# Kernel tuning notes

Hardware: AMD Instinct MI355X
Metric: run time of the kernel (lower is better)

Reference implementation:

```python
import jax, jax.numpy as jnp
import numpy as np

N_HEAD = 16
R = 8
THRESHOLD = 0.1


def setup_inputs() -> dict:
    key = jax.random.key(0)
    k1, k2, k3 = jax.random.split(key, 3)
    B, T, C = 2, 2048, 2048
    fused_dim = 3 * C  # 2*H*D_std + C + 2*H*R with D_std+R = head_dim
    x = jax.random.normal(k1, (B, T, C), dtype=jnp.float32)
    W_attn = jax.random.normal(k2, (fused_dim, C), dtype=jnp.float32) * (1.0 / np.sqrt(C))
    W_proj = jax.random.normal(k3, (C, C), dtype=jnp.float32) * (1.0 / np.sqrt(C))
    w_std = jnp.ones((N_HEAD,), dtype=jnp.float32) * 0.5
    w_rec = jnp.ones((N_HEAD,), dtype=jnp.float32) * 0.3
    return {"x": x, "W_attn": W_attn, "W_proj": W_proj, "w_std": w_std, "w_rec": w_rec}


def _causal_attention(Q, K, V):
    # Q,K: [B,H,T,D]; V: [B,H,T,Dv]; scale = 1/sqrt(D) (torch SDPA default)
    D = Q.shape[-1]
    scores = jnp.einsum("bhqd,bhkd->bhqk", Q, K) / jnp.sqrt(jnp.asarray(D, Q.dtype))
    T = Q.shape[2]
    causal = jnp.tril(jnp.ones((T, T), dtype=bool))
    scores = jnp.where(causal, scores, jnp.asarray(-jnp.inf, scores.dtype))
    probs = jax.nn.softmax(scores, axis=-1)
    return jnp.einsum("bhqk,bhkd->bhqd", probs, V)


def reference(x, W_attn, W_proj, w_std, w_rec):
    B, T, C = x.shape
    H = N_HEAD
    head_dim = C // H
    D_std = head_dim - R
    q_std_end = H * D_std
    k_std_end = q_std_end + H * D_std
    v_end = k_std_end + C
    q_low_end = v_end + H * R

    fused = jnp.einsum("btc,fc->btf", x, W_attn)  # c_attn, no bias

    def split_heads(a, d):
        return a.reshape(B, T, H, d).transpose(0, 2, 1, 3)  # [B,H,T,d]

    Q_std = split_heads(fused[..., :q_std_end], D_std)
    K_std = split_heads(fused[..., q_std_end:k_std_end], D_std)
    V = split_heads(fused[..., k_std_end:v_end], head_dim)
    Q_low = split_heads(fused[..., v_end:q_low_end], R)
    K_low = split_heads(fused[..., q_low_end:], R)

    # per-head routing: RA heads fold low-rank K/Q cross terms, baseline heads keep standard concat
    use_ra = (w_rec > THRESHOLD).reshape(1, H, 1, 1)
    ws = jnp.sqrt(jnp.clip(w_std, 1e-8, None)).reshape(1, H, 1, 1)
    wr = jnp.sqrt(jnp.clip(w_rec, 1e-8, None)).reshape(1, H, 1, 1)

    Qf_low = jnp.where(use_ra, wr * K_low, ws * Q_low)
    Kf_low = jnp.where(use_ra, wr * Q_low, ws * K_low)
    Qf = jnp.concatenate([ws * Q_std, Qf_low], axis=-1)  # [B,H,T,head_dim]
    Kf = jnp.concatenate([ws * K_std, Kf_low], axis=-1)

    out = _causal_attention(Qf, Kf, V)  # [B,H,T,head_dim]
    out = out.transpose(0, 2, 1, 3).reshape(B, T, C)
    return jnp.einsum("btc,oc->bto", out, W_proj)
```

## Files before the change

kernel.cpp:

```cpp
#include <hip/hip_runtime.h>
#include <math.h>

#define Bb 2
#define Tt 2048
#define Cc 2048
#define Hh 16
#define DH 128
#define FUSED 6144
#define Mm 4096
#define QSC 0.08838834764831845f

typedef __bf16 bf16x8 __attribute__((ext_vector_type(8)));
typedef float  f32x4  __attribute__((ext_vector_type(4)));

__device__ __forceinline__ unsigned short f2bf(float f) {
  unsigned int u = __float_as_uint(f);
  u = (u + 0x7fffu + ((u >> 16) & 1u)) >> 16;
  return (unsigned short)u;
}

__device__ __forceinline__ void gload16(const void* src, void* lds) {
  __builtin_amdgcn_global_load_lds((const __attribute__((address_space(1))) void*)src,
                                   (__attribute__((address_space(3))) void*)lds, 16, 0, 0);
}

__global__ void f2bf_arr(const float* __restrict__ src, unsigned short* __restrict__ dst, int n)
{
  int i = (blockIdx.x * blockDim.x + threadIdx.x) * 4;
  int stride = gridDim.x * blockDim.x * 4;
  for (; i < n; i += stride) {
    float4 v = *(const float4*)&src[i];
    ushort4 o;
    o.x = f2bf(v.x); o.y = f2bf(v.y); o.z = f2bf(v.z); o.w = f2bf(v.w);
    *(ushort4*)&dst[i] = o;
  }
}

template <int MODE>
__global__ __launch_bounds__(256)
void gemm_bf16(const unsigned short* __restrict__ A, const unsigned short* __restrict__ Bw,
               float* __restrict__ out,
               unsigned short* __restrict__ Qb, unsigned short* __restrict__ Kb,
               unsigned short* __restrict__ Vb,
               const float* __restrict__ w_std, const float* __restrict__ w_rec,
               int N, int K)
{
  __shared__ unsigned short As[128 * 64];
  __shared__ unsigned short Bs[128 * 64];
  __shared__ float lws[Hh], lwr[Hh];
  __shared__ int   lra[Hh];

  const int tid  = threadIdx.x;
  const int lane = tid & 63;
  const int w    = tid >> 6;
  const int wr   = w >> 1, wc = w & 1;
  const int lrow = lane & 15, lgrp = lane >> 4;
  const int m0 = blockIdx.y * 128;
  const int n0 = blockIdx.x * 128;

  if (MODE == 1 && tid < Hh) {
    float a = w_std[tid]; lws[tid] = sqrtf(a < 1e-8f ? 1e-8f : a);
    float r = w_rec[tid]; lwr[tid] = sqrtf(r < 1e-8f ? 1e-8f : r);
    lra[tid] = (r > 0.1f) ? 1 : 0;
  }

  f32x4 acc[4][4] = {};

  for (int kt = 0; kt < K; kt += 64) {
#pragma unroll
    for (int c = 0; c < 4; ++c) {
      int base16 = (c * 4 + w) * 64;
      int o16 = base16 + lane;
      int rr = o16 >> 3, cc = o16 & 7;
      int csw = (cc ^ (rr & 7)) << 3;
      gload16(A  + (size_t)(m0 + rr) * K + kt + csw, As + base16 * 8);
      gload16(Bw + (size_t)(n0 + rr) * K + kt + csw, Bs + base16 * 8);
    }
    __syncthreads();

#pragma unroll
    for (int s = 0; s < 2; ++s) {
      bf16x8 af[4], bfr[4];
#pragma unroll
      for (int i = 0; i < 4; ++i) {
        int row = wr * 64 + i * 16 + lrow;
        int ch  = s * 4 + lgrp;
        af[i]  = *(const bf16x8*)&As[row * 64 + ((ch ^ (row & 7)) << 3)];
        int col = wc * 64 + i * 16 + lrow;
        bfr[i] = *(const bf16x8*)&Bs[col * 64 + ((ch ^ (col & 7)) << 3)];
      }
#pragma unroll
      for (int i = 0; i < 4; ++i)
#pragma unroll
        for (int j = 0; j < 4; ++j)
          acc[i][j] = __builtin_amdgcn_mfma_f32_16x16x32_bf16(af[i], bfr[j], acc[i][j], 0, 0, 0);
    }
    __syncthreads();
  }

  if (MODE == 0) {
#pragma unroll
    for (int i = 0; i < 4; ++i)
#pragma unroll
      for (int r = 0; r < 4; ++r) {
        int m = m0 + wr * 64 + i * 16 + lgrp * 4 + r;
#pragma unroll
        for (int j = 0; j < 4; ++j) {
          int n = n0 + wc * 64 + j * 16 + lrow;
          out[(size_t)m * N + n] = acc[i][j][r];
        }
      }
  } else {
#pragma unroll
    for (int i = 0; i < 4; ++i)
#pragma unroll
      for (int r = 0; r < 4; ++r) {
        int m = m0 + wr * 64 + i * 16 + lgrp * 4 + r;
        int b = m >> 11, t = m & 2047;
#pragma unroll
        for (int j = 0; j < 4; ++j) {
          int f = n0 + wc * 64 + j * 16 + lrow;
          float v = acc[i][j][r];
          unsigned short* dst; int h, d; float sc;
          if (f < 1920)      { h = f / 120; d = f - h * 120; dst = Qb; sc = lws[h] * QSC; }
          else if (f < 3840) { int g = f - 1920; h = g / 120; d = g - h * 120; dst = Kb; sc = lws[h]; }
          else if (f < 5888) { int g = f - 3840; h = g >> 7; d = g & 127; dst = Vb; sc = 1.f; }
          else if (f < 6016) { int g = f - 5888; h = g >> 3; d = 120 + (g & 7);
                               if (lra[h]) { dst = Kb; sc = lwr[h]; }
                               else        { dst = Qb; sc = lws[h] * QSC; } }
          else               { int g = f - 6016; h = g >> 3; d = 120 + (g & 7);
                               if (lra[h]) { dst = Qb; sc = lwr[h] * QSC; }
                               else        { dst = Kb; sc = lws[h]; } }
          dst[((((size_t)b * Hh + h) * Tt + t) << 7) + d] = f2bf(v * sc);
        }
      }
  }
}

__global__ __launch_bounds__(256)
void vtrans(const unsigned short* __restrict__ Vb, unsigned short* __restrict__ Vtb)
{
  __shared__ unsigned short Vs[64 * 128];
  const int tid = threadIdx.x;
  const int bh = blockIdx.y, t0 = blockIdx.x * 64;
  const unsigned short* src = Vb + ((size_t)bh * Tt + t0) * DH;
#pragma unroll
  for (int c = 0; c < 4; ++c) {
    int u = c * 256 + tid;
    int row = u >> 4, ch = u & 15;
    *(uint4*)&Vs[row * 128 + ch * 8] = *(const uint4*)&src[(size_t)row * DH + ch * 8];
  }
  __syncthreads();
  unsigned short* dstb = Vtb + (size_t)bh * DH * Tt + t0;
#pragma unroll
  for (int c = 0; c < 4; ++c) {
    int u = c * 256 + tid;
    int d = u & 127, tc = u >> 7;
    unsigned short tmp[8];
#pragma unroll
    for (int j = 0; j < 8; ++j) tmp[j] = Vs[(tc * 8 + j) * 128 + d];
    *(uint4*)&dstb[(size_t)d * Tt + tc * 8] = *(uint4*)tmp;
  }
}

__global__ __launch_bounds__(256)
void attn_mfma(const unsigned short* __restrict__ Qb, const unsigned short* __restrict__ Kb,
               const unsigned short* __restrict__ Vtb, unsigned short* __restrict__ attb)
{
  __shared__ unsigned short Kt[64 * 128];
  __shared__ unsigned short Vt[128 * 64];
  __shared__ unsigned short QP[64 * 128];

  const int tid = threadIdx.x, lane = tid & 63, w = tid >> 6;
  const int lrow = lane & 15, lgrp = lane >> 4;
  const int bh = blockIdx.y;
  const int qt = 31 - blockIdx.x;
  const int q0 = qt * 64;
  const unsigned short* Qh = Qb  + (size_t)bh * Tt * DH;
  const unsigned short* Kh = Kb  + (size_t)bh * Tt * DH;
  const unsigned short* Vh = Vtb + (size_t)bh * DH * Tt;

#pragma unroll
  for (int c = 0; c < 4; ++c) {
    int base16 = (c * 4 + w) * 64;
    int o16 = base16 + lane;
    int rr = o16 >> 4, cc = o16 & 15;
    gload16(Qh + (size_t)(q0 + rr) * DH + ((cc ^ (rr & 7)) << 3), QP + base16 * 8);
  }
  __syncthreads();

  bf16x8 qf[4];
#pragma unroll
  for (int s = 0; s < 4; ++s) {
    int row = w * 16 + lrow;
    int ch  = s * 4 + lgrp;
    qf[s] = *(const bf16x8*)&QP[row * 128 + ((ch ^ (row & 7)) << 3)];
  }
  __syncthreads();

  f32x4 o[8] = {};
  float mrun[4], lrun[4];
#pragma unroll
  for (int r = 0; r < 4; ++r) { mrun[r] = -INFINITY; lrun[r] = 0.f; }
  unsigned short* Pw = QP + w * 1024;

  for (int t = 0; t <= qt; ++t) {
    const int kv0 = t * 64;
#pragma unroll
    for (int c = 0; c < 4; ++c) {
      int base16 = (c * 4 + w) * 64;
      int o16 = base16 + lane;
      { int rr = o16 >> 4, cc = o16 & 15;
        gload16(Kh + (size_t)(kv0 + rr) * DH + ((cc ^ (rr & 7)) << 3), Kt + base16 * 8); }
      { int rr = o16 >> 3, cc = o16 & 7;
        gload16(Vh + (size_t)rr * Tt + kv0 + ((cc ^ (rr & 7)) << 3), Vt + base16 * 8); }
    }
    __syncthreads();

    f32x4 sv[4] = {};
#pragma unroll
    for (int ks = 0; ks < 4; ++ks)
#pragma unroll
      for (int j = 0; j < 4; ++j) {
        int krow = j * 16 + lrow;
        int ch   = ks * 4 + lgrp;
        bf16x8 kf = *(const bf16x8*)&Kt[krow * 128 + ((ch ^ (krow & 7)) << 3)];
        sv[j] = __builtin_amdgcn_mfma_f32_16x16x32_bf16(qf[ks], kf, sv[j], 0, 0, 0);
      }

    float sc[4];
#pragma unroll
    for (int r = 0; r < 4; ++r) {
      if (t == qt) {
        int qrow = q0 + w * 16 + lgrp * 4 + r;
#pragma unroll
        for (int j = 0; j < 4; ++j) {
          int kv = kv0 + j * 16 + lrow;
          if (kv > qrow) sv[j][r] = -INFINITY;
        }
      }
      float m_ = fmaxf(fmaxf(sv[0][r], sv[1][r]), fmaxf(sv[2][r], sv[3][r]));
      m_ = fmaxf(m_, __shfl_xor(m_, 1));
      m_ = fmaxf(m_, __shfl_xor(m_, 2));
      m_ = fmaxf(m_, __shfl_xor(m_, 4));
      m_ = fmaxf(m_, __shfl_xor(m_, 8));
      float mn = fmaxf(mrun[r], m_);
      sc[r] = __expf(mrun[r] - mn);
      mrun[r] = mn;
      float rs = 0.f;
#pragma unroll
      for (int j = 0; j < 4; ++j) {
        float p = __expf(sv[j][r] - mn);
        sv[j][r] = p;
        rs += p;
      }
      rs += __shfl_xor(rs, 1);
      rs += __shfl_xor(rs, 2);
      rs += __shfl_xor(rs, 4);
      rs += __shfl_xor(rs, 8);
      lrun[r] = lrun[r] * sc[r] + rs;
    }

#pragma unroll
    for (int n = 0; n < 8; ++n)
#pragma unroll
      for (int r = 0; r < 4; ++r) o[n][r] *= sc[r];

#pragma unroll
    for (int j = 0; j < 4; ++j)
#pragma unroll
      for (int r = 0; r < 4; ++r) {
        int row = lgrp * 4 + r;
        int col = j * 16 + lrow;
        int ch  = col >> 3;
        Pw[row * 64 + ((ch ^ (row & 7)) << 3) + (col & 7)] = f2bf(sv[j][r]);
      }

#pragma unroll
    for (int ks = 0; ks < 2; ++ks) {
      int ch = ks * 4 + lgrp;
      bf16x8 pa = *(const bf16x8*)&Pw[lrow * 64 + ((ch ^ (lrow & 7)) << 3)];
#pragma unroll
      for (int n = 0; n < 8; ++n) {
        int d = n * 16 + lrow;
        bf16x8 vf = *(const bf16x8*)&Vt[d * 64 + ((ch ^ (d & 7)) << 3)];
        o[n] = __builtin_amdgcn_mfma_f32_16x16x32_bf16(pa, vf, o[n], 0, 0, 0);
      }
    }
    __syncthreads();
  }

  const int b = bh >> 4, h = bh & 15;
#pragma unroll
  for (int r = 0; r < 4; ++r) {
    float inv = 1.f / lrun[r];
    int tg = q0 + w * 16 + lgrp * 4 + r;
    unsigned short* dst = attb + ((size_t)(b * Tt + tg) * Cc) + h * DH;
#pragma unroll
    for (int n = 0; n < 8; ++n)
      dst[n * 16 + lrow] = f2bf(o[n][r] * inv);
  }
}

extern "C" void kernel_launch(void* const* d_in, const int* in_sizes, int n_in,
                              void* d_out, int out_size, void* d_ws, size_t ws_size,
                              hipStream_t stream) {
  const float* x      = (const float*)d_in[0];
  const float* W_attn = (const float*)d_in[1];
  const float* W_proj = (const float*)d_in[2];
  const float* w_std  = (const float*)d_in[3];
  const float* w_rec  = (const float*)d_in[4];
  float* outp = (float*)d_out;

  unsigned short* wsb = (unsigned short*)d_ws;
  unsigned short* xb   = wsb;
  unsigned short* Wab  = wsb + 8388608;
  unsigned short* Wpb  = wsb + 20971520;
  unsigned short* Qb   = wsb + 25165824;
  unsigned short* Kb   = wsb + 33554432;
  unsigned short* Vb   = wsb + 41943040;
  unsigned short* Vtb  = wsb + 50331648;
  unsigned short* attb = wsb + 58720256;

  f2bf_arr<<<1024, 256, 0, stream>>>(x,      xb,  Mm * Cc);
  f2bf_arr<<<1024, 256, 0, stream>>>(W_attn, Wab, FUSED * Cc);
  f2bf_arr<<<1024, 256, 0, stream>>>(W_proj, Wpb, Cc * Cc);

  gemm_bf16<1><<<dim3(FUSED / 128, Mm / 128), dim3(256), 0, stream>>>(
      xb, Wab, nullptr, Qb, Kb, Vb, w_std, w_rec, FUSED, Cc);

  vtrans<<<dim3(Tt / 64, Bb * Hh), dim3(256), 0, stream>>>(Vb, Vtb);

  attn_mfma<<<dim3(Tt / 64, Bb * Hh), dim3(256), 0, stream>>>(Qb, Kb, Vtb, attb);

  gemm_bf16<0><<<dim3(Cc / 128, Mm / 128), dim3(256), 0, stream>>>(
      attb, Wpb, outp, nullptr, nullptr, nullptr, nullptr, nullptr, Cc, Cc);
}
```

Before: 498.1 us.

## Double-buffer attention K/V tiles, pair causal Q tiles, and fuse bf16 conversions

The attention kernel now runs 512 threads on 128-row query tiles. Each block handles a pair of tiles (qt and 15-qt) so causal work is balanced across blocks. K/V tiles are double-buffered in dynamic shared memory so the next tile's global-to-LDS load overlaps the current tile's compute, and Q fragments are read straight from global memory. The three float-to-bf16 conversion launches are merged into one kernel writing a contiguous workspace. The costs are 80KB of LDS per block, lower occupancy, and a flattened 256-block grid that maps heads to consecutive block ids.

```diff
diff --git a/kernel.cpp b/kernel.cpp
--- a/kernel.cpp
+++ b/kernel.cpp
@@ -24,12 +24,17 @@
                                    (__attribute__((address_space(3))) void*)lds, 16, 0, 0);
 }
 
-__global__ void f2bf_arr(const float* __restrict__ src, unsigned short* __restrict__ dst, int n)
+#define N1 8388608
+#define N2 12582912
+#define N3 4194304
+__global__ void f2bf_all(const float* __restrict__ s1, const float* __restrict__ s2,
+                         const float* __restrict__ s3, unsigned short* __restrict__ dst)
 {
   int i = (blockIdx.x * blockDim.x + threadIdx.x) * 4;
   int stride = gridDim.x * blockDim.x * 4;
-  for (; i < n; i += stride) {
-    float4 v = *(const float4*)&src[i];
+  for (; i < N1 + N2 + N3; i += stride) {
+    const float* src = (i < N1) ? (s1 + i) : (i < N1 + N2) ? (s2 + (i - N1)) : (s3 + (i - N1 - N2));
+    float4 v = *(const float4*)src;
     ushort4 o;
     o.x = f2bf(v.x); o.y = f2bf(v.y); o.z = f2bf(v.z); o.w = f2bf(v.w);
     *(ushort4*)&dst[i] = o;
@@ -163,142 +168,155 @@
   }
 }
 
-__global__ __launch_bounds__(256)
+__global__ __launch_bounds__(512)
 void attn_mfma(const unsigned short* __restrict__ Qb, const unsigned short* __restrict__ Kb,
                const unsigned short* __restrict__ Vtb, unsigned short* __restrict__ attb)
 {
-  __shared__ unsigned short Kt[64 * 128];
-  __shared__ unsigned short Vt[128 * 64];
-  __shared__ unsigned short QP[64 * 128];
-
-  const int tid = threadIdx.x, lane = tid & 63, w = tid >> 6;
+  extern __shared__ unsigned short smem[];
+  unsigned short* KT = smem;
+  unsigned short* VT = smem + 2 * 8192;
+  unsigned short* PB = smem + 4 * 8192;
+
+  const int tid = threadIdx.x, lane = tid & 63, wav = tid >> 6;
   const int lrow = lane & 15, lgrp = lane >> 4;
-  const int bh = blockIdx.y;
-  const int qt = 31 - blockIdx.x;
-  const int q0 = qt * 64;
+  const int bid = blockIdx.x;
+  const int xs  = bid & 7;
+  const int rem = bid >> 3;
+  const int bh  = xs + ((rem & 3) << 3);
+  const int pr  = rem >> 2;
+
   const unsigned short* Qh = Qb  + (size_t)bh * Tt * DH;
   const unsigned short* Kh = Kb  + (size_t)bh * Tt * DH;
   const unsigned short* Vh = Vtb + (size_t)bh * DH * Tt;
-
-#pragma unroll
-  for (int c = 0; c < 4; ++c) {
-    int base16 = (c * 4 + w) * 64;
-    int o16 = base16 + lane;
-    int rr = o16 >> 4, cc = o16 & 15;
-    gload16(Qh + (size_t)(q0 + rr) * DH + ((cc ^ (rr & 7)) << 3), QP + base16 * 8);
-  }
-  __syncthreads();
-
-  bf16x8 qf[4];
-#pragma unroll
-  for (int s = 0; s < 4; ++s) {
-    int row = w * 16 + lrow;
-    int ch  = s * 4 + lgrp;
-    qf[s] = *(const bf16x8*)&QP[row * 128 + ((ch ^ (row & 7)) << 3)];
-  }
-  __syncthreads();
-
-  f32x4 o[8] = {};
-  float mrun[4], lrun[4];
-#pragma unroll
-  for (int r = 0; r < 4; ++r) { mrun[r] = -INFINITY; lrun[r] = 0.f; }
-  unsigned short* Pw = QP + w * 1024;
-
-  for (int t = 0; t <= qt; ++t) {
-    const int kv0 = t * 64;
-#pragma unroll
-    for (int c = 0; c < 4; ++c) {
-      int base16 = (c * 4 + w) * 64;
+  const int b = bh >> 4, h = bh & 15;
+
+  unsigned short* Pw = PB + wav * 1024;
+
+  auto stage = [&](int buf, int kv0) {
+    unsigned short* Kd = KT + buf * 8192;
+    unsigned short* Vd = VT + buf * 8192;
+#pragma unroll
+    for (int s = 0; s < 2; ++s) {
+      int base16 = s * 512 + wav * 64;
       int o16 = base16 + lane;
       { int rr = o16 >> 4, cc = o16 & 15;
-        gload16(Kh + (size_t)(kv0 + rr) * DH + ((cc ^ (rr & 7)) << 3), Kt + base16 * 8); }
+        gload16(Kh + (size_t)(kv0 + rr) * DH + ((cc ^ (rr & 7)) << 3), Kd + base16 * 8); }
       { int rr = o16 >> 3, cc = o16 & 7;
-        gload16(Vh + (size_t)rr * Tt + kv0 + ((cc ^ (rr & 7)) << 3), Vt + base16 * 8); }
-    }
-    __syncthreads();
-
-    f32x4 sv[4] = {};
+        gload16(Vh + (size_t)rr * Tt + kv0 + ((cc ^ (rr & 7)) << 3), Vd + base16 * 8); }
+    }
+  };
+
+  int cur = 0;
+  stage(0, 0);
+
+  for (int ph = 0; ph < 2; ++ph) {
+    const int qt = ph ? (15 - pr) : pr;
+    const int q0 = qt * 128;
+    const int nt = 2 * (qt + 1);
+
+    bf16x8 qf[4];
 #pragma unroll
     for (int ks = 0; ks < 4; ++ks)
-#pragma unroll
-      for (int j = 0; j < 4; ++j) {
-        int krow = j * 16 + lrow;
-        int ch   = ks * 4 + lgrp;
-        bf16x8 kf = *(const bf16x8*)&Kt[krow * 128 + ((ch ^ (krow & 7)) << 3)];
-        sv[j] = __builtin_amdgcn_mfma_f32_16x16x32_bf16(qf[ks], kf, sv[j], 0, 0, 0);
-      }
-
-    float sc[4];
+      qf[ks] = *(const bf16x8*)(Qh + (size_t)(q0 + wav * 16 + lrow) * DH + ks * 32 + lgrp * 8);
+
+    f32x4 o[8] = {};
+    float mrun[4], lrun[4];
+#pragma unroll
+    for (int r = 0; r < 4; ++r) { mrun[r] = -INFINITY; lrun[r] = 0.f; }
+
+    for (int t = 0; t < nt; ++t) {
+      const int kv0 = t * 64;
+      __syncthreads();
+      bool more = (t + 1 < nt);
+      if (more)            stage(cur ^ 1, kv0 + 64);
+      else if (ph == 0)    stage(cur ^ 1, 0);
+
+      const unsigned short* Kc = KT + cur * 8192;
+      const unsigned short* Vc = VT + cur * 8192;
+
+      f32x4 sv[4] = {};
+#pragma unroll
+      for (int ks = 0; ks < 4; ++ks)
+#pragma unroll
+        for (int j = 0; j < 4; ++j) {
+          int krow = j * 16 + lrow;
+          int ch   = ks * 4 + lgrp;
+          bf16x8 kf = *(const bf16x8*)&Kc[krow * 128 + ((ch ^ (krow & 7)) << 3)];
+          sv[j] = __builtin_amdgcn_mfma_f32_16x16x32_bf16(qf[ks], kf, sv[j], 0, 0, 0);
+        }
+
+      const bool domask = (kv0 >= q0);
+      float sc[4];
+#pragma unroll
+      for (int r = 0; r < 4; ++r) {
+        if (domask) {
+          int qrow = q0 + wav * 16 + lgrp * 4 + r;
+#pragma unroll
+          for (int j = 0; j < 4; ++j) {
+            int kv = kv0 + j * 16 + lrow;
+            if (kv > qrow) sv[j][r] = -INFINITY;
+          }
+        }
+        float m_ = fmaxf(fmaxf(sv[0][r], sv[1][r]), fmaxf(sv[2][r], sv[3][r]));
+        m_ = fmaxf(m_, __shfl_xor(m_, 1));
+        m_ = fmaxf(m_, __shfl_xor(m_, 2));
+        m_ = fmaxf(m_, __shfl_xor(m_, 4));
+        m_ = fmaxf(m_, __shfl_xor(m_, 8));
+        float mn = fmaxf(mrun[r], m_);
+        sc[r] = __expf(mrun[r] - mn);
+        mrun[r] = mn;
+        float rs = 0.f;
+#pragma unroll
+        for (int j = 0; j < 4; ++j) {
+          float p = __expf(sv[j][r] - mn);
+          sv[j][r] = p;
+          rs += p;
+        }
+        rs += __shfl_xor(rs, 1);
+        rs += __shfl_xor(rs, 2);
+        rs += __shfl_xor(rs, 4);
+        rs += __shfl_xor(rs, 8);
+        lrun[r] = lrun[r] * sc[r] + rs;
+      }
+
+#pragma unroll
+      for (int n = 0; n < 8; ++n)
+#pragma unroll
+        for (int r = 0; r < 4; ++r) o[n][r] *= sc[r];
+
+#pragma unroll
+      for (int j = 0; j < 4; ++j)
+#pragma unroll
+        for (int r = 0; r < 4; ++r) {
+          int row = lgrp * 4 + r;
+          int col = j * 16 + lrow;
+          int ch  = col >> 3;
+          Pw[row * 64 + ((ch ^ (row & 7)) << 3) + (col & 7)] = f2bf(sv[j][r]);
+        }
+
+#pragma unroll
+      for (int ks = 0; ks < 2; ++ks) {
+        int ch = ks * 4 + lgrp;
+        bf16x8 pa = *(const bf16x8*)&Pw[lrow * 64 + ((ch ^ (lrow & 7)) << 3)];
+#pragma unroll
+        for (int n = 0; n < 8; ++n) {
+          int d = n * 16 + lrow;
+          bf16x8 vf = *(const bf16x8*)&Vc[d * 64 + ((ch ^ (d & 7)) << 3)];
+          o[n] = __builtin_amdgcn_mfma_f32_16x16x32_bf16(pa, vf, o[n], 0, 0, 0);
+        }
+      }
+      cur ^= 1;
+    }
+
 #pragma unroll
     for (int r = 0; r < 4; ++r) {
-      if (t == qt) {
-        int qrow = q0 + w * 16 + lgrp * 4 + r;
-#pragma unroll
-        for (int j = 0; j < 4; ++j) {
-          int kv = kv0 + j * 16 + lrow;
-          if (kv > qrow) sv[j][r] = -INFINITY;
-        }
-      }
-      float m_ = fmaxf(fmaxf(sv[0][r], sv[1][r]), fmaxf(sv[2][r], sv[3][r]));
-      m_ = fmaxf(m_, __shfl_xor(m_, 1));
-      m_ = fmaxf(m_, __shfl_xor(m_, 2));
-      m_ = fmaxf(m_, __shfl_xor(m_, 4));
-      m_ = fmaxf(m_, __shfl_xor(m_, 8));
-      float mn = fmaxf(mrun[r], m_);
-      sc[r] = __expf(mrun[r] - mn);
-      mrun[r] = mn;
-      float rs = 0.f;
-#pragma unroll
-      for (int j = 0; j < 4; ++j) {
-        float p = __expf(sv[j][r] - mn);
-        sv[j][r] = p;
-        rs += p;
-      }
-      rs += __shfl_xor(rs, 1);
-      rs += __shfl_xor(rs, 2);
-      rs += __shfl_xor(rs, 4);
-      rs += __shfl_xor(rs, 8);
-      lrun[r] = lrun[r] * sc[r] + rs;
-    }
-
-#pragma unroll
-    for (int n = 0; n < 8; ++n)
-#pragma unroll
-      for (int r = 0; r < 4; ++r) o[n][r] *= sc[r];
-
-#pragma unroll
-    for (int j = 0; j < 4; ++j)
-#pragma unroll
-      for (int r = 0; r < 4; ++r) {
-        int row = lgrp * 4 + r;
-        int col = j * 16 + lrow;
-        int ch  = col >> 3;
-        Pw[row * 64 + ((ch ^ (row & 7)) << 3) + (col & 7)] = f2bf(sv[j][r]);
-      }
-
-#pragma unroll
-    for (int ks = 0; ks < 2; ++ks) {
-      int ch = ks * 4 + lgrp;
-      bf16x8 pa = *(const bf16x8*)&Pw[lrow * 64 + ((ch ^ (lrow & 7)) << 3)];
-#pragma unroll
-      for (int n = 0; n < 8; ++n) {
-        int d = n * 16 + lrow;
-        bf16x8 vf = *(const bf16x8*)&Vt[d * 64 + ((ch ^ (d & 7)) << 3)];
-        o[n] = __builtin_amdgcn_mfma_f32_16x16x32_bf16(pa, vf, o[n], 0, 0, 0);
-      }
-    }
-    __syncthreads();
-  }
-
-  const int b = bh >> 4, h = bh & 15;
-#pragma unroll
-  for (int r = 0; r < 4; ++r) {
-    float inv = 1.f / lrun[r];
-    int tg = q0 + w * 16 + lgrp * 4 + r;
-    unsigned short* dst = attb + ((size_t)(b * Tt + tg) * Cc) + h * DH;
-#pragma unroll
-    for (int n = 0; n < 8; ++n)
-      dst[n * 16 + lrow] = f2bf(o[n][r] * inv);
+      float inv = 1.f / lrun[r];
+      int tg = q0 + wav * 16 + lgrp * 4 + r;
+      unsigned short* dst = attb + ((size_t)(b * Tt + tg) * Cc) + h * DH;
+#pragma unroll
+      for (int n = 0; n < 8; ++n)
+        dst[n * 16 + lrow] = f2bf(o[n][r] * inv);
+    }
   }
 }
 
@@ -322,16 +340,14 @@
   unsigned short* Vtb  = wsb + 50331648;
   unsigned short* attb = wsb + 58720256;
 
-  f2bf_arr<<<1024, 256, 0, stream>>>(x,      xb,  Mm * Cc);
-  f2bf_arr<<<1024, 256, 0, stream>>>(W_attn, Wab, FUSED * Cc);
-  f2bf_arr<<<1024, 256, 0, stream>>>(W_proj, Wpb, Cc * Cc);
+  f2bf_all<<<2048, 256, 0, stream>>>(x, W_attn, W_proj, wsb);
 
   gemm_bf16<1><<<dim3(FUSED / 128, Mm / 128), dim3(256), 0, stream>>>(
       xb, Wab, nullptr, Qb, Kb, Vb, w_std, w_rec, FUSED, Cc);
 
   vtrans<<<dim3(Tt / 64, Bb * Hh), dim3(256), 0, stream>>>(Vb, Vtb);
 
-  attn_mfma<<<dim3(Tt / 64, Bb * Hh), dim3(256), 0, stream>>>(Qb, Kb, Vtb, attb);
+  attn_mfma<<<dim3(256), dim3(512), 81920, stream>>>(Qb, Kb, Vtb, attb);
 
   gemm_bf16<0><<<dim3(Cc / 128, Mm / 128), dim3(256), 0, stream>>>(
       attb, Wpb, outp, nullptr, nullptr, nullptr, nullptr, nullptr, Cc, Cc);
```

After: 432.6 us. 13.2% less time.
